# Optimization experiments

Measured on AMD Instinct MI355X. Metric: run time of the kernel, lower is better.

## Reference

```python
import jax, jax.numpy as jnp
import numpy as np

N = 8192
F_IN = 128
F_OUT = 64
ALPHA = 0.2
NEG_INF = -9.0e15  # matches -9000000000000000.0 in the torch source


def setup_inputs() -> dict:
    key = jax.random.key(0)
    k1, k2, k3, k4 = jax.random.split(key, 4)
    h = jax.random.normal(k1, (N, F_IN), dtype=jnp.float32)
    adj = jax.random.randint(k2, (N, N), 0, 2).astype(jnp.int32)
    W = jax.random.normal(k3, (F_IN, F_OUT), dtype=jnp.float32) * 0.05
    a = jax.random.normal(k4, (2 * F_OUT,), dtype=jnp.float32) * 0.05
    return {"h": h, "adj": adj, "W": W, "a": a}


def reference(h, adj, W, a):
    # Wh: [N, F_OUT]
    Wh = h @ W
    # a([Wh_i ; Wh_j]) == Wh_i @ a1 + Wh_j @ a2 -> avoid O(N^2*2F) concat
    a1, a2 = a[:F_OUT], a[F_OUT:]
    s_src = Wh @ a1  # [N] contribution of row node i
    s_dst = Wh @ a2  # [N] contribution of col node j
    e = jax.nn.leaky_relu(s_src[:, None] + s_dst[None, :], negative_slope=ALPHA)  # [N, N]
    e = jnp.where(adj > 0, e, NEG_INF)
    attention = jax.nn.softmax(e, axis=1)  # [N, N]
    h_prime = attention @ Wh  # [N, F_OUT]
    return jax.nn.elu(h_prime)
```

## Files before the change

### kernel.cpp

```cpp
#include <hip/hip_runtime.h>
#include <hip/hip_bf16.h>

#define N 8192
#define FIN 128
#define FOUT 64
#define CSPLIT 2
#define CHUNK (N / CSPLIT)
#define M 32
#define TILE 128
#define NT (CHUNK / TILE)

typedef __attribute__((ext_vector_type(4))) float f32x4;
typedef __attribute__((ext_vector_type(4))) int i32x4;
typedef __attribute__((ext_vector_type(8))) short bf16x8;

#define GLOAD_LDS16(gp, lp)                                                    \
    __builtin_amdgcn_global_load_lds(                                          \
        (const __attribute__((address_space(1))) void*)(gp),                   \
        (__attribute__((address_space(3))) void*)(lp), 16, 0, 0)

__device__ __forceinline__ short f2bf(float x) {
    __hip_bfloat16 b = __float2bfloat16(x);
    union { __hip_bfloat16 b; short s; } u; u.b = b; return u.s;
}

__global__ __launch_bounds__(256) void wh_kernel(
    const float* __restrict__ h, const float* __restrict__ W,
    const float* __restrict__ a,
    __hip_bfloat16* __restrict__ whT, float* __restrict__ s_src,
    float* __restrict__ s_dst) {
    const int wave = threadIdx.x >> 6;
    const int lane = threadIdx.x & 63;
    const int row = blockIdx.x * 4 + wave;
    const float* hr = h + (size_t)row * FIN;
    float acc = 0.f;
#pragma unroll 8
    for (int k = 0; k < FIN; ++k) {
        acc += hr[k] * W[k * FOUT + lane];
    }
    whT[(size_t)lane * N + row] = __float2bfloat16(acc);
    float s1 = acc * a[lane];
    float s2 = acc * a[FOUT + lane];
#pragma unroll
    for (int mm = 32; mm >= 1; mm >>= 1) {
        s1 += __shfl_xor(s1, mm, 64);
        s2 += __shfl_xor(s2, mm, 64);
    }
    if (lane == 0) { s_src[row] = s1; s_dst[row] = s2; }
}

__global__ __launch_bounds__(512, 4) void gat_partial(
    const int* __restrict__ adj, const __hip_bfloat16* __restrict__ whT,
    const float* __restrict__ s_src, const float* __restrict__ s_dst,
    float* __restrict__ numP, float* __restrict__ denP) {
    union SMem {
        struct {
            int adjb[2][M][TILE];
            short whb[2][FOUT][TILE];
            float sdl[CHUNK];
        } s;
        struct { float pC[4][M][FOUT]; float pD[4][M]; } e;
    };
    __shared__ SMem sm;

    const int tid = threadIdx.x;
    const int w = tid >> 6, lane = tid & 63;
    const int m = lane & 15, kg = lane >> 4;
    const int wr = w >> 2, wc = w & 3;
    const int rg = blockIdx.x >> 1;
    const int c = blockIdx.x & 1;
    const int ibase = rg * M;
    const int cb = c * CHUNK;
    const float ssrc = s_src[ibase + wr * 16 + m];
    const int sidx = w * 2;

    f32x4 acc[4] = {{0,0,0,0},{0,0,0,0},{0,0,0,0},{0,0,0,0}};
    float dsum = 0.f;

    auto stage = [&](int t, int buf) {
        const int gcol = cb + t * TILE;
#pragma unroll
        for (int q = 0; q < 2; ++q) {
            const int idx = sidx + q;
            const int r = idx * 2 + (lane >> 5);
            const int b = ((lane & 31) * 16) ^ ((r & 31) << 4);
            GLOAD_LDS16(adj + (size_t)(ibase + r) * N + gcol + (b >> 2),
                        &sm.s.adjb[buf][idx * 2][0]);
        }
#pragma unroll
        for (int q = 0; q < 2; ++q) {
            const int idx = sidx + q;
            const int f = idx * 4 + (lane >> 4);
            const int b = ((lane & 15) * 16) ^ ((f & 15) << 4);
            GLOAD_LDS16(whT + (size_t)f * N + gcol + (b >> 1),
                        &sm.s.whb[buf][idx * 4][0]);
        }
    };

#pragma unroll
    for (int q = 0; q < 2; ++q) {
        const int idx = sidx + q;
        GLOAD_LDS16(s_dst + cb + idx * 256 + lane * 4, &sm.s.sdl[idx * 256]);
    }
    stage(0, 0);
    stage(1, 1);
    asm volatile("s_waitcnt vmcnt(4)" ::: "memory");
    __builtin_amdgcn_s_barrier();

#pragma unroll 2
    for (int t = 0; t < NT; ++t) {
        const int buf = t & 1;

        {
            const int kcol = wc * 32 + kg * 8;
            const int aRow = wr * 16 + m;
            const char* adjbase = (const char*)&sm.s.adjb[buf][0][0];
            const int aswz = (aRow & 31) << 4;
            i32x4 a0 = *(const i32x4*)(adjbase + aRow * 512 + ((kcol * 4) ^ aswz));
            i32x4 a1 = *(const i32x4*)(adjbase + aRow * 512 + ((kcol * 4 + 16) ^ aswz));
            f32x4 d0 = *(const f32x4*)&sm.s.sdl[t * TILE + kcol];
            f32x4 d1 = *(const f32x4*)&sm.s.sdl[t * TILE + kcol + 4];
            const char* whbase = (const char*)&sm.s.whb[buf][0][0];
            bf16x8 bq0 = *(const bf16x8*)(whbase + (0 * 16 + m) * 256 + ((kcol * 2) ^ (m << 4)));
            bf16x8 bq1 = *(const bf16x8*)(whbase + (1 * 16 + m) * 256 + ((kcol * 2) ^ (m << 4)));
            bf16x8 bq2 = *(const bf16x8*)(whbase + (2 * 16 + m) * 256 + ((kcol * 2) ^ (m << 4)));
            bf16x8 bq3 = *(const bf16x8*)(whbase + (3 * 16 + m) * 256 + ((kcol * 2) ^ (m << 4)));

            bf16x8 afr;
#pragma unroll
            for (int e = 0; e < 4; ++e) {
                float x = ssrc + d0[e];
                x = (x >= 0.f) ? x : 0.2f * x;
                float p = (a0[e] != 0) ? __expf(x) : 0.f;
                dsum += p;
                afr[e] = f2bf(p);
            }
#pragma unroll
            for (int e = 0; e < 4; ++e) {
                float x = ssrc + d1[e];
                x = (x >= 0.f) ? x : 0.2f * x;
                float p = (a1[e] != 0) ? __expf(x) : 0.f;
                dsum += p;
                afr[4 + e] = f2bf(p);
            }

            acc[0] = __builtin_amdgcn_mfma_f32_16x16x32_bf16(afr, bq0, acc[0], 0, 0, 0);
            acc[1] = __builtin_amdgcn_mfma_f32_16x16x32_bf16(afr, bq1, acc[1], 0, 0, 0);
            acc[2] = __builtin_amdgcn_mfma_f32_16x16x32_bf16(afr, bq2, acc[2], 0, 0, 0);
            acc[3] = __builtin_amdgcn_mfma_f32_16x16x32_bf16(afr, bq3, acc[3], 0, 0, 0);
        }

        __builtin_amdgcn_s_barrier();
        if (t + 2 < NT) {
            stage(t + 2, buf);
            asm volatile("s_waitcnt vmcnt(4)" ::: "memory");
            __builtin_amdgcn_s_barrier();
        } else if (t + 1 < NT) {
            asm volatile("s_waitcnt vmcnt(0)" ::: "memory");
            __builtin_amdgcn_s_barrier();
        }
    }

    dsum += __shfl_xor(dsum, 16, 64);
    dsum += __shfl_xor(dsum, 32, 64);

#pragma unroll
    for (int r = 0; r < 4; ++r) {
#pragma unroll
        for (int q = 0; q < 4; ++q) {
            sm.e.pC[wc][wr * 16 + kg * 4 + r][q * 16 + m] = acc[q][r];
        }
    }
    if (kg == 0) sm.e.pD[wc][wr * 16 + m] = dsum;
    __syncthreads();

    float* numC = numP + (size_t)c * N * FOUT;
    float* denC = denP + (size_t)c * N;
#pragma unroll
    for (int k = 0; k < 4; ++k) {
        int idx = k * 512 + tid;
        int i = idx >> 6, f = idx & 63;
        float num = sm.e.pC[0][i][f] + sm.e.pC[1][i][f] + sm.e.pC[2][i][f] + sm.e.pC[3][i][f];
        numC[(size_t)(ibase + i) * FOUT + f] = num;
        if (f == 0) {
            denC[ibase + i] = sm.e.pD[0][i] + sm.e.pD[1][i] + sm.e.pD[2][i] + sm.e.pD[3][i];
        }
    }
}

__global__ __launch_bounds__(256) void gat_combine(
    const float* __restrict__ numP, const float* __restrict__ denP,
    float* __restrict__ out) {
    int idx = blockIdx.x * 256 + threadIdx.x;
    int row = idx >> 6;
    float num = 0.f, den = 0.f;
#pragma unroll
    for (int cc = 0; cc < CSPLIT; ++cc) {
        num += numP[(size_t)cc * N * FOUT + idx];
        den += denP[(size_t)cc * N + row];
    }
    float v = num / den;
    out[idx] = (v > 0.f) ? v : expm1f(v);
}

extern "C" void kernel_launch(void* const* d_in, const int* in_sizes, int n_in,
                              void* d_out, int out_size, void* d_ws, size_t ws_size,
                              hipStream_t stream) {
    const float* h = (const float*)d_in[0];
    const int* adj = (const int*)d_in[1];
    const float* W = (const float*)d_in[2];
    const float* a = (const float*)d_in[3];
    float* out = (float*)d_out;

    char* ws = (char*)d_ws;
    __hip_bfloat16* whT = (__hip_bfloat16*)ws;
    float* s_src = (float*)(ws + (size_t)FOUT * N * sizeof(__hip_bfloat16));
    float* s_dst = s_src + N;
    float* numP = s_dst + N;
    float* denP = numP + (size_t)CSPLIT * N * FOUT;

    hipLaunchKernelGGL(wh_kernel, dim3(N / 4), dim3(256), 0, stream,
                       h, W, a, whT, s_src, s_dst);
    hipLaunchKernelGGL(gat_partial, dim3((N / M) * CSPLIT), dim3(512), 0, stream,
                       adj, whT, s_src, s_dst, numP, denP);
    hipLaunchKernelGGL(gat_combine, dim3(N * FOUT / 256), dim3(256), 0, stream,
                       numP, denP, out);
}
```

Measured before the change: 88.54 us.

## Pre-pack adjacency into bitmask and stage W in LDS for Wh

```diff
diff --git a/kernel.cpp b/kernel.cpp
--- a/kernel.cpp
+++ b/kernel.cpp
@@ -24,19 +24,55 @@
     union { __hip_bfloat16 b; short s; } u; u.b = b; return u.s;
 }
 
+__global__ __launch_bounds__(256) void pack_kernel(
+    const int* __restrict__ adj, unsigned int* __restrict__ pk) {
+    const int w = threadIdx.x >> 6, lane = threadIdx.x & 63;
+    const int gw = blockIdx.x * 4 + w;
+#pragma unroll 4
+    for (int it = 0; it < 32; ++it) {
+        const int task = it * 8192 + gw;
+        const int rr = task >> 5;
+        const int gg = task & 31;
+        i32x4 v = *(const i32x4*)(adj + (size_t)rr * N + gg * 256 + lane * 4);
+        unsigned nib = (v[0] != 0 ? 1u : 0u) | (v[1] != 0 ? 2u : 0u) |
+                       (v[2] != 0 ? 4u : 0u) | (v[3] != 0 ? 8u : 0u);
+        unsigned u;
+        u = (unsigned)__shfl_xor((int)nib, 1, 64); nib |= u << 4;
+        u = (unsigned)__shfl_xor((int)nib, 2, 64); nib |= u << 8;
+        u = (unsigned)__shfl_xor((int)nib, 4, 64); nib |= u << 16;
+        if ((lane & 7) == 0) {
+            const int wi = gg * 8 + (lane >> 3);
+            pk[(size_t)rr * 256 + (wi ^ (rr & 7))] = nib;
+        }
+    }
+}
+
 __global__ __launch_bounds__(256) void wh_kernel(
     const float* __restrict__ h, const float* __restrict__ W,
     const float* __restrict__ a,
     __hip_bfloat16* __restrict__ whT, float* __restrict__ s_src,
     float* __restrict__ s_dst) {
-    const int wave = threadIdx.x >> 6;
+    __shared__ float Wl[FIN * FOUT];
+    const int w = threadIdx.x >> 6;
     const int lane = threadIdx.x & 63;
-    const int row = blockIdx.x * 4 + wave;
+#pragma unroll
+    for (int q = 0; q < 8; ++q) {
+        const int i = w * 8 + q;
+        GLOAD_LDS16(W + i * 256 + lane * 4, &Wl[i * 256]);
+    }
+    asm volatile("s_waitcnt vmcnt(0)" ::: "memory");
+    __syncthreads();
+
+    const int row = blockIdx.x * 4 + w;
     const float* hr = h + (size_t)row * FIN;
     float acc = 0.f;
-#pragma unroll 8
-    for (int k = 0; k < FIN; ++k) {
-        acc += hr[k] * W[k * FOUT + lane];
+#pragma unroll
+    for (int k0 = 0; k0 < FIN; k0 += 4) {
+        f32x4 hv = *(const f32x4*)(hr + k0);
+        acc += hv[0] * Wl[(k0 + 0) * FOUT + lane];
+        acc += hv[1] * Wl[(k0 + 1) * FOUT + lane];
+        acc += hv[2] * Wl[(k0 + 2) * FOUT + lane];
+        acc += hv[3] * Wl[(k0 + 3) * FOUT + lane];
     }
     whT[(size_t)lane * N + row] = __float2bfloat16(acc);
     float s1 = acc * a[lane];
@@ -50,14 +86,14 @@
 }
 
 __global__ __launch_bounds__(512, 4) void gat_partial(
-    const int* __restrict__ adj, const __hip_bfloat16* __restrict__ whT,
+    const unsigned int* __restrict__ pkg, const __hip_bfloat16* __restrict__ whT,
     const float* __restrict__ s_src, const float* __restrict__ s_dst,
     float* __restrict__ numP, float* __restrict__ denP) {
     union SMem {
         struct {
-            int adjb[2][M][TILE];
+            unsigned int pkl[M][CHUNK / 32];
+            float sdl[CHUNK];
             short whb[2][FOUT][TILE];
-            float sdl[CHUNK];
         } s;
         struct { float pC[4][M][FOUT]; float pD[4][M]; } e;
     };
@@ -71,22 +107,15 @@
     const int c = blockIdx.x & 1;
     const int ibase = rg * M;
     const int cb = c * CHUNK;
-    const float ssrc = s_src[ibase + wr * 16 + m];
+    const int aRow = wr * 16 + m;
+    const float ssrc = s_src[ibase + aRow];
     const int sidx = w * 2;
 
     f32x4 acc[4] = {{0,0,0,0},{0,0,0,0},{0,0,0,0},{0,0,0,0}};
     float dsum = 0.f;
 
-    auto stage = [&](int t, int buf) {
+    auto stageWh = [&](int t, int buf) {
         const int gcol = cb + t * TILE;
-#pragma unroll
-        for (int q = 0; q < 2; ++q) {
-            const int idx = sidx + q;
-            const int r = idx * 2 + (lane >> 5);
-            const int b = ((lane & 31) * 16) ^ ((r & 31) << 4);
-            GLOAD_LDS16(adj + (size_t)(ibase + r) * N + gcol + (b >> 2),
-                        &sm.s.adjb[buf][idx * 2][0]);
-        }
 #pragma unroll
         for (int q = 0; q < 2; ++q) {
             const int idx = sidx + q;
@@ -99,25 +128,28 @@
 
 #pragma unroll
     for (int q = 0; q < 2; ++q) {
-        const int idx = sidx + q;
-        GLOAD_LDS16(s_dst + cb + idx * 256 + lane * 4, &sm.s.sdl[idx * 256]);
-    }
-    stage(0, 0);
-    stage(1, 1);
-    asm volatile("s_waitcnt vmcnt(4)" ::: "memory");
+        const int i = sidx + q;
+        const int r = 2 * i + (lane >> 5);
+        GLOAD_LDS16(pkg + (size_t)(ibase + r) * 256 + c * 128 + (lane & 31) * 4,
+                    &sm.s.pkl[2 * i][0]);
+    }
+#pragma unroll
+    for (int q = 0; q < 2; ++q) {
+        const int i = sidx + q;
+        GLOAD_LDS16(s_dst + cb + i * 256 + lane * 4, &sm.s.sdl[i * 256]);
+    }
+    stageWh(0, 0);
+    stageWh(1, 1);
+    asm volatile("s_waitcnt vmcnt(2)" ::: "memory");
     __builtin_amdgcn_s_barrier();
 
 #pragma unroll 2
     for (int t = 0; t < NT; ++t) {
         const int buf = t & 1;
-
         {
             const int kcol = wc * 32 + kg * 8;
-            const int aRow = wr * 16 + m;
-            const char* adjbase = (const char*)&sm.s.adjb[buf][0][0];
-            const int aswz = (aRow & 31) << 4;
-            i32x4 a0 = *(const i32x4*)(adjbase + aRow * 512 + ((kcol * 4) ^ aswz));
-            i32x4 a1 = *(const i32x4*)(adjbase + aRow * 512 + ((kcol * 4 + 16) ^ aswz));
+            const unsigned int pw = sm.s.pkl[aRow][(t * 4 + wc) ^ (aRow & 7)];
+            const unsigned int tq = (pw >> (kg * 8)) & 0xffu;
             f32x4 d0 = *(const f32x4*)&sm.s.sdl[t * TILE + kcol];
             f32x4 d1 = *(const f32x4*)&sm.s.sdl[t * TILE + kcol + 4];
             const char* whbase = (const char*)&sm.s.whb[buf][0][0];
@@ -131,7 +163,7 @@
             for (int e = 0; e < 4; ++e) {
                 float x = ssrc + d0[e];
                 x = (x >= 0.f) ? x : 0.2f * x;
-                float p = (a0[e] != 0) ? __expf(x) : 0.f;
+                float p = ((tq >> e) & 1u) ? __expf(x) : 0.f;
                 dsum += p;
                 afr[e] = f2bf(p);
             }
@@ -139,7 +171,7 @@
             for (int e = 0; e < 4; ++e) {
                 float x = ssrc + d1[e];
                 x = (x >= 0.f) ? x : 0.2f * x;
-                float p = (a1[e] != 0) ? __expf(x) : 0.f;
+                float p = ((tq >> (4 + e)) & 1u) ? __expf(x) : 0.f;
                 dsum += p;
                 afr[4 + e] = f2bf(p);
             }
@@ -152,8 +184,8 @@
 
         __builtin_amdgcn_s_barrier();
         if (t + 2 < NT) {
-            stage(t + 2, buf);
-            asm volatile("s_waitcnt vmcnt(4)" ::: "memory");
+            stageWh(t + 2, buf);
+            asm volatile("s_waitcnt vmcnt(2)" ::: "memory");
             __builtin_amdgcn_s_barrier();
         } else if (t + 1 < NT) {
             asm volatile("s_waitcnt vmcnt(0)" ::: "memory");
@@ -218,11 +250,13 @@
     float* s_dst = s_src + N;
     float* numP = s_dst + N;
     float* denP = numP + (size_t)CSPLIT * N * FOUT;
-
+    unsigned int* pk = (unsigned int*)(denP + (size_t)CSPLIT * N);
+
+    hipLaunchKernelGGL(pack_kernel, dim3(2048), dim3(256), 0, stream, adj, pk);
     hipLaunchKernelGGL(wh_kernel, dim3(N / 4), dim3(256), 0, stream,
                        h, W, a, whT, s_src, s_dst);
     hipLaunchKernelGGL(gat_partial, dim3((N / M) * CSPLIT), dim3(512), 0, stream,
-                       adj, whT, s_src, s_dst, numP, denP);
+                       pk, whT, s_src, s_dst, numP, denP);
     hipLaunchKernelGGL(gat_combine, dim3(N * FOUT / 256), dim3(256), 0, stream,
                        numP, denP, out);
 }
```

Result: slower. 96.77 us (+9.3%).

## Fold log2e into scores, use raw exp2, packed bf16 cvt, MFMA row-sum denominator

Applied to the files above, without the earlier changes.

```diff
diff --git a/kernel.cpp b/kernel.cpp
--- a/kernel.cpp
+++ b/kernel.cpp
@@ -9,6 +9,7 @@
 #define M 32
 #define TILE 128
 #define NT (CHUNK / TILE)
+#define LOG2E 1.44269504f
 
 typedef __attribute__((ext_vector_type(4))) float f32x4;
 typedef __attribute__((ext_vector_type(4))) int i32x4;
@@ -18,25 +19,33 @@
     __builtin_amdgcn_global_load_lds(                                          \
         (const __attribute__((address_space(1))) void*)(gp),                   \
         (__attribute__((address_space(3))) void*)(lp), 16, 0, 0)
-
-__device__ __forceinline__ short f2bf(float x) {
-    __hip_bfloat16 b = __float2bfloat16(x);
-    union { __hip_bfloat16 b; short s; } u; u.b = b; return u.s;
-}
 
 __global__ __launch_bounds__(256) void wh_kernel(
     const float* __restrict__ h, const float* __restrict__ W,
     const float* __restrict__ a,
     __hip_bfloat16* __restrict__ whT, float* __restrict__ s_src,
     float* __restrict__ s_dst) {
-    const int wave = threadIdx.x >> 6;
+    __shared__ float Wl[FIN * FOUT];
+    const int w = threadIdx.x >> 6;
     const int lane = threadIdx.x & 63;
-    const int row = blockIdx.x * 4 + wave;
+#pragma unroll
+    for (int q = 0; q < 8; ++q) {
+        const int i = w * 8 + q;
+        GLOAD_LDS16(W + i * 256 + lane * 4, &Wl[i * 256]);
+    }
+    asm volatile("s_waitcnt vmcnt(0)" ::: "memory");
+    __syncthreads();
+
+    const int row = blockIdx.x * 4 + w;
     const float* hr = h + (size_t)row * FIN;
     float acc = 0.f;
-#pragma unroll 8
-    for (int k = 0; k < FIN; ++k) {
-        acc += hr[k] * W[k * FOUT + lane];
+#pragma unroll
+    for (int k0 = 0; k0 < FIN; k0 += 4) {
+        f32x4 hv = *(const f32x4*)(hr + k0);
+        acc += hv[0] * Wl[(k0 + 0) * FOUT + lane];
+        acc += hv[1] * Wl[(k0 + 1) * FOUT + lane];
+        acc += hv[2] * Wl[(k0 + 2) * FOUT + lane];
+        acc += hv[3] * Wl[(k0 + 3) * FOUT + lane];
     }
     whT[(size_t)lane * N + row] = __float2bfloat16(acc);
     float s1 = acc * a[lane];
@@ -46,7 +55,7 @@
         s1 += __shfl_xor(s1, mm, 64);
         s2 += __shfl_xor(s2, mm, 64);
     }
-    if (lane == 0) { s_src[row] = s1; s_dst[row] = s2; }
+    if (lane == 0) { s_src[row] = s1 * LOG2E; s_dst[row] = s2 * LOG2E; }
 }
 
 __global__ __launch_bounds__(512, 4) void gat_partial(
@@ -71,11 +80,14 @@
     const int c = blockIdx.x & 1;
     const int ibase = rg * M;
     const int cb = c * CHUNK;
-    const float ssrc = s_src[ibase + wr * 16 + m];
+    const int aRow = wr * 16 + m;
+    const float ssrc = s_src[ibase + aRow];
     const int sidx = w * 2;
 
     f32x4 acc[4] = {{0,0,0,0},{0,0,0,0},{0,0,0,0},{0,0,0,0}};
-    float dsum = 0.f;
+    f32x4 acc4 = {0,0,0,0};
+    const short oneb = (m == 0) ? (short)0x3F80 : (short)0;
+    const bf16x8 bones = {oneb, oneb, oneb, oneb, oneb, oneb, oneb, oneb};
 
     auto stage = [&](int t, int buf) {
         const int gcol = cb + t * TILE;
@@ -113,7 +125,6 @@
 
         {
             const int kcol = wc * 32 + kg * 8;
-            const int aRow = wr * 16 + m;
             const char* adjbase = (const char*)&sm.s.adjb[buf][0][0];
             const int aswz = (aRow & 31) << 4;
             i32x4 a0 = *(const i32x4*)(adjbase + aRow * 512 + ((kcol * 4) ^ aswz));
@@ -126,28 +137,35 @@
             bf16x8 bq2 = *(const bf16x8*)(whbase + (2 * 16 + m) * 256 + ((kcol * 2) ^ (m << 4)));
             bf16x8 bq3 = *(const bf16x8*)(whbase + (3 * 16 + m) * 256 + ((kcol * 2) ^ (m << 4)));
 
-            bf16x8 afr;
+            float p[8];
 #pragma unroll
             for (int e = 0; e < 4; ++e) {
                 float x = ssrc + d0[e];
-                x = (x >= 0.f) ? x : 0.2f * x;
-                float p = (a0[e] != 0) ? __expf(x) : 0.f;
-                dsum += p;
-                afr[e] = f2bf(p);
+                float xl = fmaxf(x, 0.2f * x);
+                float pe;
+                asm("v_exp_f32 %0, %1" : "=v"(pe) : "v"(xl));
+                p[e] = (a0[e] != 0) ? pe : 0.f;
             }
 #pragma unroll
             for (int e = 0; e < 4; ++e) {
                 float x = ssrc + d1[e];
-                x = (x >= 0.f) ? x : 0.2f * x;
-                float p = (a1[e] != 0) ? __expf(x) : 0.f;
-                dsum += p;
-                afr[4 + e] = f2bf(p);
+                float xl = fmaxf(x, 0.2f * x);
+                float pe;
+                asm("v_exp_f32 %0, %1" : "=v"(pe) : "v"(xl));
+                p[4 + e] = (a1[e] != 0) ? pe : 0.f;
             }
-
-            acc[0] = __builtin_amdgcn_mfma_f32_16x16x32_bf16(afr, bq0, acc[0], 0, 0, 0);
-            acc[1] = __builtin_amdgcn_mfma_f32_16x16x32_bf16(afr, bq1, acc[1], 0, 0, 0);
-            acc[2] = __builtin_amdgcn_mfma_f32_16x16x32_bf16(afr, bq2, acc[2], 0, 0, 0);
-            acc[3] = __builtin_amdgcn_mfma_f32_16x16x32_bf16(afr, bq3, acc[3], 0, 0, 0);
+            union { bf16x8 v; unsigned u[4]; } afr;
+#pragma unroll
+            for (int q = 0; q < 4; ++q) {
+                asm("v_cvt_pk_bf16_f32 %0, %1, %2"
+                    : "=v"(afr.u[q]) : "v"(p[2 * q]), "v"(p[2 * q + 1]));
+            }
+
+            acc[0] = __builtin_amdgcn_mfma_f32_16x16x32_bf16(afr.v, bq0, acc[0], 0, 0, 0);
+            acc[1] = __builtin_amdgcn_mfma_f32_16x16x32_bf16(afr.v, bq1, acc[1], 0, 0, 0);
+            acc[2] = __builtin_amdgcn_mfma_f32_16x16x32_bf16(afr.v, bq2, acc[2], 0, 0, 0);
+            acc[3] = __builtin_amdgcn_mfma_f32_16x16x32_bf16(afr.v, bq3, acc[3], 0, 0, 0);
+            acc4   = __builtin_amdgcn_mfma_f32_16x16x32_bf16(afr.v, bones, acc4, 0, 0, 0);
         }
 
         __builtin_amdgcn_s_barrier();
@@ -161,9 +179,6 @@
         }
     }
 
-    dsum += __shfl_xor(dsum, 16, 64);
-    dsum += __shfl_xor(dsum, 32, 64);
-
 #pragma unroll
     for (int r = 0; r < 4; ++r) {
 #pragma unroll
@@ -171,7 +186,12 @@
             sm.e.pC[wc][wr * 16 + kg * 4 + r][q * 16 + m] = acc[q][r];
         }
     }
-    if (kg == 0) sm.e.pD[wc][wr * 16 + m] = dsum;
+    if (m == 0) {
+#pragma unroll
+        for (int r = 0; r < 4; ++r) {
+            sm.e.pD[wc][wr * 16 + kg * 4 + r] = acc4[r];
+        }
+    }
     __syncthreads();
 
     float* numC = numP + (size_t)c * N * FOUT;
```

After: 80.67 us. 8.9% less time.
